# Kernel optimization log

Measured on AMD Instinct MI355X. Metric: run time of the kernel, lower is better.

## Reference

```python
import jax, jax.numpy as jnp
import numpy as np


def setup_inputs() -> dict:
    key = jax.random.key(0)
    k1, k2 = jax.random.split(key)
    B, C, H, W = 4, 256, 128, 128
    x1 = jax.random.normal(k1, (B, C, H, W), dtype=jnp.float32)
    x2 = jax.random.normal(k2, (B, C, H, W), dtype=jnp.float32)
    return {"x1": x1, "x2": x2, "d": 4}


def reference(x1, x2, d):
    # Windowed correlation cost volume: for each offset (i,j) in a
    # (2d+1)x(2d+1) window, mean over channels of x1 * shifted(x2).
    B, C, H, W = x1.shape
    out_dim = 2 * d + 1
    x2p = jnp.pad(x2, ((0, 0), (0, 0), (d, d), (d, d)))  # [B,C,H+2d,W+2d]
    inv_c = jnp.asarray(1.0 / C, dtype=x1.dtype)
    # Fixed small loop over 81 structural offsets; each term fuses
    # multiply + channel-sum.
    cv = [
        jnp.sum(x1 * jax.lax.dynamic_slice(x2p, (0, 0, i, j), (B, C, H, W)), axis=1) * inv_c
        for i in range(out_dim)
        for j in range(out_dim)
    ]
    return jnp.stack(cv, axis=1)  # [B, (2d+1)^2, H, W]
```

## Files before the change

### kernel.cpp

```cpp
#include <hip/hip_runtime.h>

namespace {

constexpr int Cn   = 256;
constexpr int Hh   = 128;
constexpr int Ww   = 128;
constexpr int HW   = Hh * Ww;
constexpr int TILE = 16;
constexpr int CCH  = 8;
constexpr int NCH  = Cn / CCH;
constexpr int HALO = 4;
constexpr int X2T  = 24;
constexpr int X2S  = 24;
constexpr int X2CH = X2T * X2S;
constexpr int X1CH = TILE * TILE;
constexpr int NOFF = 81;


__device__ __forceinline__ void gl2lds16(const float* g, float* l) {
  __builtin_amdgcn_global_load_lds(
      (const __attribute__((address_space(1))) void*)g,
      (__attribute__((address_space(3))) void*)l, 16, 0, 0);
}

__global__ __launch_bounds__(576, 1)
void costvol_kernel(const float* __restrict__ x1,
                    const float* __restrict__ x2,
                    const float* __restrict__ zp,
                    float* __restrict__ out)
{
  __shared__ float sx2[2][CCH * X2CH];
  __shared__ float sx1[2][CCH * X1CH];

  const int t    = threadIdx.x;
  const int wv   = t >> 6;
  const int lane = t & 63;
  const int h    = lane >> 2;
  const int m    = lane & 3;

  const int tx = blockIdx.x, ty = blockIdx.y, b = blockIdx.z;
  const int x0 = tx * TILE, y0 = ty * TILE;

  const float* g2 = x2 + (size_t)b * Cn * HW;

  const float* gp0;  size_t inc0;
  const float* gp1;  size_t inc1;
  {
    const int s = t, ch = s / 144, rem = s % 144, row = rem / 6, c4 = rem % 6;
    const int gy = y0 - HALO + row, gx = x0 - HALO + 4 * c4;
    const bool ok = ((unsigned)gy < (unsigned)Hh) && (gx >= 0) && (gx + 3 < Ww);
    gp0  = ok ? (g2 + (size_t)ch * HW + (size_t)gy * Ww + gx) : zp;
    inc0 = ok ? (size_t)(CCH * HW) : 0;
  }
  {
    const int s = t + 576, ch = s / 144, rem = s % 144, row = rem / 6, c4 = rem % 6;
    const int gy = y0 - HALO + row, gx = x0 - HALO + 4 * c4;
    const bool ok = ((unsigned)gy < (unsigned)Hh) && (gx >= 0) && (gx + 3 < Ww);
    gp1  = ok ? (g2 + (size_t)ch * HW + (size_t)gy * Ww + gx) : zp;
    inc1 = ok ? (size_t)(CCH * HW) : 0;
  }
  const int lds0 = (t >> 6) * 256;
  const int lds1 = lds0 + 9 * 256;

  const float* gpx;  size_t incx;
  if (wv < 8) {
    gpx  = x1 + (size_t)b * Cn * HW + (size_t)wv * HW
             + (size_t)(y0 + h) * Ww + (x0 + 4 * m);
    incx = (size_t)(CCH * HW);
  } else {
    gpx  = zp;
    incx = 0;
  }
  const int ldsx = wv * X1CH;

  float acc[9][4];
#pragma unroll
  for (int d = 0; d < 9; ++d)
#pragma unroll
    for (int p = 0; p < 4; ++p) acc[d][p] = 0.0f;

  const int rbase = (h + wv) * X2S + 4 * m;
  const int abase = h * TILE + 4 * m;

  auto quad = [&](int hc, const float* sc, const float* s1c) {
    float4 a[4];
    float  w[4][12];
#pragma unroll
    for (int cc = 0; cc < 4; ++cc) {
      a[cc] = *reinterpret_cast<const float4*>(s1c + (4 * hc + cc) * X1CH + abase);
      const float* bp = sc + (4 * hc + cc) * X2CH + rbase;
      *reinterpret_cast<float4*>(w[cc])     = *reinterpret_cast<const float4*>(bp);
      *reinterpret_cast<float4*>(w[cc] + 4) = *reinterpret_cast<const float4*>(bp + 4);
      *reinterpret_cast<float4*>(w[cc] + 8) = *reinterpret_cast<const float4*>(bp + 8);
    }
#pragma unroll
    for (int cc = 0; cc < 4; ++cc)
#pragma unroll
      for (int dj = 0; dj < 9; ++dj) {
        acc[dj][0] = fmaf(a[cc].x, w[cc][dj + 0], acc[dj][0]);
        acc[dj][1] = fmaf(a[cc].y, w[cc][dj + 1], acc[dj][1]);
        acc[dj][2] = fmaf(a[cc].z, w[cc][dj + 2], acc[dj][2]);
        acc[dj][3] = fmaf(a[cc].w, w[cc][dj + 3], acc[dj][3]);
      }
  };

  auto stage = [&](int nb) {
    gl2lds16(gp0, &sx2[nb][lds0]);  gp0 += inc0;
    gl2lds16(gp1, &sx2[nb][lds1]);  gp1 += inc1;
    if (wv < 8) { gl2lds16(gpx, &sx1[nb][ldsx]);  gpx += incx; }
  };

  stage(0);
  asm volatile("s_waitcnt vmcnt(0)" ::: "memory");
  __syncthreads();

  for (int k = 0; k < NCH; ++k) {
    if (k + 1 < NCH) stage((k + 1) & 1);
    const float* sc  = sx2[k & 1];
    const float* s1c = sx1[k & 1];
    quad(0, sc, s1c);
    quad(1, sc, s1c);
    asm volatile("s_waitcnt vmcnt(0)" ::: "memory");
    __syncthreads();
  }

  const float invc = 1.0f / (float)Cn;
  const int y  = y0 + h;
  const int xb = x0 + 4 * m;
#pragma unroll
  for (int dj = 0; dj < 9; ++dj) {
    const int o = wv * 9 + dj;
    float4 v;
    v.x = acc[dj][0] * invc;
    v.y = acc[dj][1] * invc;
    v.z = acc[dj][2] * invc;
    v.w = acc[dj][3] * invc;
    *reinterpret_cast<float4*>(out + (((size_t)b * NOFF + o) * Hh + y) * Ww + xb) = v;
  }
}

}

extern "C" void kernel_launch(void* const* d_in, const int* in_sizes, int n_in,
                              void* d_out, int out_size, void* d_ws, size_t ws_size,
                              hipStream_t stream) {
  const float* x1 = (const float*)d_in[0];
  const float* x2 = (const float*)d_in[1];
  float* out = (float*)d_out;

  hipMemsetAsync(d_ws, 0, 256, stream);

  dim3 grid(Ww / TILE, Hh / TILE, 4);
  dim3 block(576);
  costvol_kernel<<<grid, block, 0, stream>>>(x1, x2, (const float*)d_ws, out);
}
```

Baseline: 80.64 us.

## Load x1 directly from global, widen per-thread tile, split channels across half-waves

Drops the LDS staging buffer for x1. Each lane now reads its x1 values straight from global memory as two float4 loads per channel. The per-thread work changes from 4 output columns over all 8 staged channels to 8 output columns over 4 channels, with the two half-waves covering different channel halves. A cross-lane shuffle reduction combines the halves at the end. The aim is less LDS traffic and fewer LDS loads per FMA, but it adds register pressure (72 accumulators) and exposes uncached global-load latency inside the compute loop.

Measured after the change: 113.6 us. 40.9% more time.

```diff
diff --git a/kernel.cpp b/kernel.cpp
--- a/kernel.cpp
+++ b/kernel.cpp
@@ -13,7 +13,6 @@
 constexpr int X2T  = 24;
 constexpr int X2S  = 24;
 constexpr int X2CH = X2T * X2S;
-constexpr int X1CH = TILE * TILE;
 constexpr int NOFF = 81;
 
 
@@ -30,18 +29,20 @@
                     float* __restrict__ out)
 {
   __shared__ float sx2[2][CCH * X2CH];
-  __shared__ float sx1[2][CCH * X1CH];
 
-  const int t    = threadIdx.x;
-  const int wv   = t >> 6;
-  const int lane = t & 63;
-  const int h    = lane >> 2;
-  const int m    = lane & 3;
+  const int t  = threadIdx.x;
+  const int wv = t >> 6;
+  const int l  = t & 63;
+  const int h  = l & 15;
+  const int m2 = (l >> 4) & 1;
+  const int c2 = l >> 5;
 
   const int tx = blockIdx.x, ty = blockIdx.y, b = blockIdx.z;
   const int x0 = tx * TILE, y0 = ty * TILE;
 
   const float* g2 = x2 + (size_t)b * Cn * HW;
+  const float* g1 = x1 + (size_t)b * Cn * HW + (size_t)(4 * c2) * HW
+                       + (size_t)(y0 + h) * Ww + (x0 + 8 * m2);
 
   const float* gp0;  size_t inc0;
   const float* gp1;  size_t inc1;
@@ -62,52 +63,40 @@
   const int lds0 = (t >> 6) * 256;
   const int lds1 = lds0 + 9 * 256;
 
-  const float* gpx;  size_t incx;
-  if (wv < 8) {
-    gpx  = x1 + (size_t)b * Cn * HW + (size_t)wv * HW
-             + (size_t)(y0 + h) * Ww + (x0 + 4 * m);
-    incx = (size_t)(CCH * HW);
-  } else {
-    gpx  = zp;
-    incx = 0;
-  }
-  const int ldsx = wv * X1CH;
+  auto stage = [&](int nb) {
+    gl2lds16(gp0, &sx2[nb][lds0]);  gp0 += inc0;
+    gl2lds16(gp1, &sx2[nb][lds1]);  gp1 += inc1;
+  };
 
-  float acc[9][4];
+  float acc[9][8];
 #pragma unroll
   for (int d = 0; d < 9; ++d)
 #pragma unroll
-    for (int p = 0; p < 4; ++p) acc[d][p] = 0.0f;
+    for (int p = 0; p < 8; ++p) acc[d][p] = 0.0f;
 
-  const int rbase = (h + wv) * X2S + 4 * m;
-  const int abase = h * TILE + 4 * m;
+  const int rbase = (h + wv) * X2S + 8 * m2;
 
-  auto quad = [&](int hc, const float* sc, const float* s1c) {
-    float4 a[4];
-    float  w[4][12];
+  auto chan = [&](int k, int cc, const float* sc) {
+    const float* ga = g1 + (size_t)(k * CCH + cc) * HW;
+    const float4 a0 = *reinterpret_cast<const float4*>(ga);
+    const float4 a1 = *reinterpret_cast<const float4*>(ga + 4);
+    const float* bp = sc + (4 * c2 + cc) * X2CH + rbase;
+    float w[16];
+    *reinterpret_cast<float4*>(w)      = *reinterpret_cast<const float4*>(bp);
+    *reinterpret_cast<float4*>(w + 4)  = *reinterpret_cast<const float4*>(bp + 4);
+    *reinterpret_cast<float4*>(w + 8)  = *reinterpret_cast<const float4*>(bp + 8);
+    *reinterpret_cast<float4*>(w + 12) = *reinterpret_cast<const float4*>(bp + 12);
 #pragma unroll
-    for (int cc = 0; cc < 4; ++cc) {
-      a[cc] = *reinterpret_cast<const float4*>(s1c + (4 * hc + cc) * X1CH + abase);
-      const float* bp = sc + (4 * hc + cc) * X2CH + rbase;
-      *reinterpret_cast<float4*>(w[cc])     = *reinterpret_cast<const float4*>(bp);
-      *reinterpret_cast<float4*>(w[cc] + 4) = *reinterpret_cast<const float4*>(bp + 4);
-      *reinterpret_cast<float4*>(w[cc] + 8) = *reinterpret_cast<const float4*>(bp + 8);
+    for (int dj = 0; dj < 9; ++dj) {
+      acc[dj][0] = fmaf(a0.x, w[dj + 0], acc[dj][0]);
+      acc[dj][1] = fmaf(a0.y, w[dj + 1], acc[dj][1]);
+      acc[dj][2] = fmaf(a0.z, w[dj + 2], acc[dj][2]);
+      acc[dj][3] = fmaf(a0.w, w[dj + 3], acc[dj][3]);
+      acc[dj][4] = fmaf(a1.x, w[dj + 4], acc[dj][4]);
+      acc[dj][5] = fmaf(a1.y, w[dj + 5], acc[dj][5]);
+      acc[dj][6] = fmaf(a1.z, w[dj + 6], acc[dj][6]);
+      acc[dj][7] = fmaf(a1.w, w[dj + 7], acc[dj][7]);
     }
-#pragma unroll
-    for (int cc = 0; cc < 4; ++cc)
-#pragma unroll
-      for (int dj = 0; dj < 9; ++dj) {
-        acc[dj][0] = fmaf(a[cc].x, w[cc][dj + 0], acc[dj][0]);
-        acc[dj][1] = fmaf(a[cc].y, w[cc][dj + 1], acc[dj][1]);
-        acc[dj][2] = fmaf(a[cc].z, w[cc][dj + 2], acc[dj][2]);
-        acc[dj][3] = fmaf(a[cc].w, w[cc][dj + 3], acc[dj][3]);
-      }
-  };
-
-  auto stage = [&](int nb) {
-    gl2lds16(gp0, &sx2[nb][lds0]);  gp0 += inc0;
-    gl2lds16(gp1, &sx2[nb][lds1]);  gp1 += inc1;
-    if (wv < 8) { gl2lds16(gpx, &sx1[nb][ldsx]);  gpx += incx; }
   };
 
   stage(0);
@@ -116,26 +105,40 @@
 
   for (int k = 0; k < NCH; ++k) {
     if (k + 1 < NCH) stage((k + 1) & 1);
-    const float* sc  = sx2[k & 1];
-    const float* s1c = sx1[k & 1];
-    quad(0, sc, s1c);
-    quad(1, sc, s1c);
+    const float* sc = sx2[k & 1];
+    chan(k, 0, sc);
+    chan(k, 1, sc);
+    chan(k, 2, sc);
+    chan(k, 3, sc);
     asm volatile("s_waitcnt vmcnt(0)" ::: "memory");
     __syncthreads();
   }
 
-  const float invc = 1.0f / (float)Cn;
-  const int y  = y0 + h;
-  const int xb = x0 + 4 * m;
 #pragma unroll
-  for (int dj = 0; dj < 9; ++dj) {
-    const int o = wv * 9 + dj;
-    float4 v;
-    v.x = acc[dj][0] * invc;
-    v.y = acc[dj][1] * invc;
-    v.z = acc[dj][2] * invc;
-    v.w = acc[dj][3] * invc;
-    *reinterpret_cast<float4*>(out + (((size_t)b * NOFF + o) * Hh + y) * Ww + xb) = v;
+  for (int dj = 0; dj < 9; ++dj)
+#pragma unroll
+    for (int p = 0; p < 8; ++p) {
+      float v = acc[dj][p];
+      v += __shfl_down(v, 32);
+      acc[dj][p] = v;
+    }
+
+  if (l < 32) {
+    const float invc = 1.0f / (float)Cn;
+    const int y  = y0 + h;
+    const int xb = x0 + 8 * m2;
+#pragma unroll
+    for (int dj = 0; dj < 9; ++dj) {
+      const int o = wv * 9 + dj;
+      float* op = out + (((size_t)b * NOFF + o) * Hh + y) * Ww + xb;
+      float4 v0, v1;
+      v0.x = acc[dj][0] * invc; v0.y = acc[dj][1] * invc;
+      v0.z = acc[dj][2] * invc; v0.w = acc[dj][3] * invc;
+      v1.x = acc[dj][4] * invc; v1.y = acc[dj][5] * invc;
+      v1.z = acc[dj][6] * invc; v1.w = acc[dj][7] * invc;
+      *reinterpret_cast<float4*>(op)     = v0;
+      *reinterpret_cast<float4*>(op + 4) = v1;
+    }
   }
 }
 
```

## Triple-buffer LDS staging with partial vmcnt waits to deepen prefetch

Applied to the files above, without the earlier changes.

Moves from double to triple buffering of the x1/x2 channel chunks in LDS, prefetching two chunks ahead. Each iteration waits only for the oldest outstanding loads (vmcnt(3)) instead of draining all of them. The conditional x1 load is made uniform by routing idle waves into a dummy LDS region. The goal is to hide global-load latency behind compute, at the cost of more LDS use and possible race risk from the lighter barrier and waitcnt handling.

After: 107.8 us. 33.6% more time.

```diff
diff --git a/kernel.cpp b/kernel.cpp
--- a/kernel.cpp
+++ b/kernel.cpp
@@ -29,8 +29,9 @@
                     const float* __restrict__ zp,
                     float* __restrict__ out)
 {
-  __shared__ float sx2[2][CCH * X2CH];
-  __shared__ float sx1[2][CCH * X1CH];
+  __shared__ float sx2[3][CCH * X2CH];
+  __shared__ float sx1[3][CCH * X1CH];
+  __shared__ float dump[64 * 4];
 
   const int t    = threadIdx.x;
   const int wv   = t >> 6;
@@ -62,16 +63,28 @@
   const int lds0 = (t >> 6) * 256;
   const int lds1 = lds0 + 9 * 256;
 
-  const float* gpx;  size_t incx;
+  const float* gpx;  size_t incx;  float* x1base;  int x1str;
   if (wv < 8) {
-    gpx  = x1 + (size_t)b * Cn * HW + (size_t)wv * HW
-             + (size_t)(y0 + h) * Ww + (x0 + 4 * m);
-    incx = (size_t)(CCH * HW);
+    gpx    = x1 + (size_t)b * Cn * HW + (size_t)wv * HW
+                + (size_t)(y0 + h) * Ww + (x0 + 4 * m);
+    incx   = (size_t)(CCH * HW);
+    x1base = &sx1[0][wv * X1CH];
+    x1str  = CCH * X1CH;
   } else {
-    gpx  = zp;
-    incx = 0;
+    gpx    = zp;
+    incx   = 0;
+    x1base = dump;
+    x1str  = 0;
   }
-  const int ldsx = wv * X1CH;
+
+  float* const sx2f = &sx2[0][0];
+  float* const sx1f = &sx1[0][0];
+
+  auto stage = [&](int nb) {
+    gl2lds16(gp0, sx2f + nb * (CCH * X2CH) + lds0);  gp0 += inc0;
+    gl2lds16(gp1, sx2f + nb * (CCH * X2CH) + lds1);  gp1 += inc1;
+    gl2lds16(gpx, x1base + nb * x1str);              gpx += incx;
+  };
 
   float acc[9][4];
 #pragma unroll
@@ -104,24 +117,25 @@
       }
   };
 
-  auto stage = [&](int nb) {
-    gl2lds16(gp0, &sx2[nb][lds0]);  gp0 += inc0;
-    gl2lds16(gp1, &sx2[nb][lds1]);  gp1 += inc1;
-    if (wv < 8) { gl2lds16(gpx, &sx1[nb][ldsx]);  gpx += incx; }
-  };
-
   stage(0);
-  asm volatile("s_waitcnt vmcnt(0)" ::: "memory");
-  __syncthreads();
+  stage(1);
+  asm volatile("s_waitcnt vmcnt(3)" ::: "memory");
+  __builtin_amdgcn_s_barrier();
+  __builtin_amdgcn_sched_barrier(0);
 
   for (int k = 0; k < NCH; ++k) {
-    if (k + 1 < NCH) stage((k + 1) & 1);
-    const float* sc  = sx2[k & 1];
-    const float* s1c = sx1[k & 1];
+    if (k + 2 < NCH) stage((k + 2) % 3);
+    const float* sc  = sx2f + (k % 3) * (CCH * X2CH);
+    const float* s1c = sx1f + (k % 3) * (CCH * X1CH);
     quad(0, sc, s1c);
     quad(1, sc, s1c);
-    asm volatile("s_waitcnt vmcnt(0)" ::: "memory");
-    __syncthreads();
+    if (k + 2 < NCH) {
+      asm volatile("s_waitcnt vmcnt(3)" ::: "memory");
+    } else {
+      asm volatile("s_waitcnt vmcnt(0)" ::: "memory");
+    }
+    __builtin_amdgcn_s_barrier();
+    __builtin_amdgcn_sched_barrier(0);
   }
 
   const float invc = 1.0f / (float)Cn;
```
